# Optimization experiments

Hardware: AMD Instinct MI355X
Metric: run time of the kernel (lower is better)

## Reference

```python
import jax, jax.numpy as jnp
import numpy as np

B, L, D = 32, 256, 1024
ALIGN = 1024
FF = 2048
NUM_CLASSES = 3


def setup_inputs() -> dict:
    key = jax.random.key(0)
    ks = jax.random.split(key, 10)
    u = lambda k, shape: jax.random.uniform(k, shape, jnp.float32, -1.0, 1.0)
    return {
        "premises": jax.random.normal(ks[0], (B, L, D), jnp.float32),
        "hypotheses": jax.random.normal(ks[1], (B, L, D), jnp.float32),
        "W_F": u(ks[2], (D, ALIGN)),
        "W_G": u(ks[3], (2 * D, FF)),
        "W1": u(ks[4], (2 * FF, FF)) * 0.02,
        "b1": jnp.zeros((FF,), jnp.float32),
        "W2": u(ks[5], (FF, FF)) * 0.02,
        "b2": jnp.zeros((FF,), jnp.float32),
        "W3": u(ks[6], (FF, NUM_CLASSES)) * 0.02,
        "b3": jnp.zeros((NUM_CLASSES,), jnp.float32),
    }


def reference(premises, hypotheses, W_F, W_G, W1, b1, W2, b2, W3, b3):
    # ---- align: tanh-projected cross attention ----
    F_p = jnp.tanh(jnp.einsum("bpd,da->bpa", premises, W_F))      # [B,Lp,A]
    F_h = jnp.tanh(jnp.einsum("bhd,da->bha", hypotheses, W_F))    # [B,Lh,A]
    eijs = jnp.einsum("bpa,bha->bph", F_p, F_h)                   # [B,Lp,Lh]
    attn = jax.nn.softmax(eijs, axis=-1)                          # tf.nn.softmax: last axis
    betas = jnp.einsum("bph,bhd->bpd", attn, hypotheses)          # [B,Lp,D]
    alphas = jnp.einsum("bph,bpd->bhd", attn, premises)           # [B,Lh,D]

    # ---- compare (dropout is identity: p_keep = 1.0 at eval) ----
    V1 = jnp.tanh(jnp.concatenate([premises, betas], axis=2) @ W_G)    # [B,Lp,FF]
    V2 = jnp.tanh(jnp.concatenate([hypotheses, alphas], axis=2) @ W_G) # [B,Lh,FF]

    # ---- aggregate: sum-pool over sequence, concat ----
    agg = jnp.concatenate([V1.sum(axis=1), V2.sum(axis=1)], axis=1)    # [B,2*FF]

    # ---- classifier MLP ----
    a1 = jnp.tanh(agg @ W1 + b1)
    a2 = jnp.tanh(a1 @ W2 + b2)
    logits = a2 @ W3 + b3                                              # [B,3]
    return logits
```

## Files before the change

kernel.cpp:

```cpp
#include <hip/hip_runtime.h>
#include <hip/hip_bf16.h>
#include <stdint.h>


typedef __attribute__((ext_vector_type(8))) short    short8_t;
typedef __attribute__((ext_vector_type(4))) float    float4_t;
typedef __attribute__((ext_vector_type(8))) _Float16 half8_t;
typedef __attribute__((ext_vector_type(4))) _Float16 half4_t;
typedef __attribute__((ext_vector_type(2))) _Float16 half2_t;

#define DEVI static __device__ __forceinline__

DEVI short f2bf(float f) {
  union { float f; unsigned u; } v; v.f = f;
  unsigned r = v.u + 0x7fffu + ((v.u >> 16) & 1u);
  return (short)(r >> 16);
}
DEVI float bf2f(short s) {
  union { unsigned u; float f; } v;
  v.u = ((unsigned)(unsigned short)s) << 16;
  return v.f;
}
DEVI void split2(float x, short& hi, short& lo) {
  hi = f2bf(x);
  lo = f2bf(x - bf2f(hi));
}
DEVI float fast_tanh(float x) {
  float e = __expf(2.0f * x);
  return 1.0f - 2.0f / (e + 1.0f);
}
DEVI void gload16(const void* g, void* l) {
  __builtin_amdgcn_global_load_lds(
      (const __attribute__((address_space(1))) void*)g,
      (__attribute__((address_space(3))) void*)l, 16, 0, 0);
}

__global__ __launch_bounds__(512, 2) void gemm_split_f(
    const short* __restrict__ Ah, const short* __restrict__ Al,
    const short* __restrict__ Bh, const short* __restrict__ Bl,
    short* __restrict__ Fh, short* __restrict__ Fl)
{
  __shared__ __align__(16) short LDS[3][24576];

  const int id   = blockIdx.x;
  const int row0 = (id >> 2) * 128;
  const int col0 = (id & 3) * 256;
  const int tid  = threadIdx.x;
  const int lane = tid & 63, wave = tid >> 6;
  const int wr = wave >> 2, wc = wave & 3;
  const int m15 = lane & 15, q = lane >> 4;
  const int nt = 1024 / 32;

  const int cg = ((lane & 3) ^ ((lane >> 3) & 3)) * 8;
  const short* gptr[6];
  int ldsoff[6];
#pragma unroll
  for (int c = 0; c < 6; ++c) {
    const int f0 = wave * 96 + c * 16;
    const int fr = f0 + (lane >> 2);
    const short* base;
    size_t roff;
    if (f0 < 128)      { base = Ah; roff = (size_t)(row0 + fr) * 1024; }
    else if (f0 < 256) { base = Al; roff = (size_t)(row0 + fr - 128) * 1024; }
    else if (f0 < 512) { base = Bh; roff = (size_t)(col0 + fr - 256) * 1024; }
    else               { base = Bl; roff = (size_t)(col0 + fr - 512) * 1024; }
    gptr[c]   = base + roff + cg;
    ldsoff[c] = f0 * 32;
  }
  auto stage = [&](short* slotbase, int kt) {
#pragma unroll
    for (int c = 0; c < 6; ++c)
      gload16(gptr[c] + kt * 32, slotbase + ldsoff[c]);
  };

  const int xq = (q ^ ((m15 >> 1) & 3)) * 8;
  int arow[4], brow[4];
#pragma unroll
  for (int i = 0; i < 4; ++i) {
    arow[i] = (wr * 64 + i * 16 + m15) * 32 + xq;
    brow[i] = 8192 + (wc * 64 + i * 16 + m15) * 32 + xq;
  }

  float4_t acc[4][4];
#pragma unroll
  for (int i = 0; i < 4; ++i)
#pragma unroll
    for (int j = 0; j < 4; ++j) acc[i][j] = (float4_t)0.0f;

  stage(&LDS[0][0], 0);
  stage(&LDS[1][0], 1);
  asm volatile("s_waitcnt vmcnt(6)");
  __builtin_amdgcn_s_barrier();

  int cur = 0, st2 = 2;
  for (int t = 0; t < nt; ++t) {
    short* buf = &LDS[cur][0];
    __builtin_amdgcn_sched_barrier(0);

    short8_t ah[4], al[4], bh[4], bl[4];
#pragma unroll
    for (int i = 0; i < 4; ++i) {
      ah[i] = *(const short8_t*)&buf[arow[i]];
      al[i] = *(const short8_t*)&buf[arow[i] + 4096];
    }
#pragma unroll
    for (int j = 0; j < 4; ++j) {
      bh[j] = *(const short8_t*)&buf[brow[j]];
      bl[j] = *(const short8_t*)&buf[brow[j] + 8192];
    }

    if (t + 2 < nt) stage(&LDS[st2][0], t + 2);

    __builtin_amdgcn_s_setprio(1);
#pragma unroll
    for (int i = 0; i < 4; ++i)
#pragma unroll
      for (int j = 0; j < 4; ++j) {
        acc[i][j] = __builtin_amdgcn_mfma_f32_16x16x32_bf16(ah[i], bh[j], acc[i][j], 0, 0, 0);
        acc[i][j] = __builtin_amdgcn_mfma_f32_16x16x32_bf16(ah[i], bl[j], acc[i][j], 0, 0, 0);
        acc[i][j] = __builtin_amdgcn_mfma_f32_16x16x32_bf16(al[i], bh[j], acc[i][j], 0, 0, 0);
      }
    __builtin_amdgcn_s_setprio(0);

    __builtin_amdgcn_sched_barrier(0);
    if (t + 2 < nt) {
      asm volatile("s_waitcnt vmcnt(6)");
    } else if (t + 1 < nt) {
      asm volatile("s_waitcnt vmcnt(0)");
    }
    __builtin_amdgcn_s_barrier();
    cur = (cur == 2) ? 0 : cur + 1;
    st2 = (st2 == 2) ? 0 : st2 + 1;
  }

#pragma unroll
  for (int i = 0; i < 4; ++i) {
#pragma unroll
    for (int r = 0; r < 4; ++r) {
      const int gm = row0 + wr * 64 + i * 16 + q * 4 + r;
#pragma unroll
      for (int j = 0; j < 4; ++j) {
        const int gn = col0 + wc * 64 + j * 16 + m15;
        float v = fast_tanh(acc[i][j][r]);
        short hi, lo; split2(v, hi, lo);
        Fh[(size_t)gm * 1024 + gn] = hi;
        Fl[(size_t)gm * 1024 + gn] = lo;
      }
    }
  }
}

template <int DO_TANH, int OUT_MODE>
__global__ __launch_bounds__(256) void gemm_nt_split(
    const short* __restrict__ Ah, const short* __restrict__ Al, int lda, long sA,
    const short* __restrict__ Bh, const short* __restrict__ Bl, int ldb, long sB,
    void* __restrict__ Ch, void* __restrict__ Cl, int ldc, long sC,
    int M, int K, int kslices)
{
  __shared__ __align__(16) short Ash[128 * 32];
  __shared__ __align__(16) short Asl[128 * 32];
  __shared__ __align__(16) short Bsh[128 * 32];
  __shared__ __align__(16) short Bsl[128 * 32];

  const int z  = blockIdx.z;
  const int zb = z / kslices;
  const int Ksub = K / kslices;
  const int zk = z - zb * kslices;
  const int kbeg = zk * Ksub, kend = kbeg + Ksub;

  Ah += (size_t)zb * sA;  Al += (size_t)zb * sA;
  Bh += (size_t)zb * sB;  Bl += (size_t)zb * sB;

  const int row0 = blockIdx.x * 128;
  const int col0 = blockIdx.y * 128;

  const int t    = threadIdx.x;
  const int lane = t & 63;
  const int wave = t >> 6;
  const int wr = wave >> 1, wc = wave & 1;
  const int m15 = lane & 15, q = lane >> 4;

  const int schk = ((t & 3) ^ ((t >> 3) & 3)) * 8;
  const short* pAh = Ah + (size_t)(row0 + (t >> 2)) * lda + kbeg + schk;
  const short* pAl = Al + (size_t)(row0 + (t >> 2)) * lda + kbeg + schk;
  const short* pBh = Bh + (size_t)(col0 + (t >> 2)) * ldb + kbeg + schk;
  const short* pBl = Bl + (size_t)(col0 + (t >> 2)) * ldb + kbeg + schk;
  const size_t a64 = (size_t)64 * lda, b64 = (size_t)64 * ldb;
  short* lAh = &Ash[wave * 512];
  short* lAl = &Asl[wave * 512];
  short* lBh = &Bsh[wave * 512];
  short* lBl = &Bsl[wave * 512];

  const int fs2 = (q ^ ((m15 >> 1) & 3)) * 8;

  float4_t acc[4][4];
#pragma unroll
  for (int i = 0; i < 4; ++i)
#pragma unroll
    for (int j = 0; j < 4; ++j) acc[i][j] = (float4_t)0.0f;

  for (int k0 = kbeg; k0 < kend; k0 += 32) {
    gload16(pAh, lAh);  gload16(pAh + a64, lAh + 2048);
    gload16(pAl, lAl);  gload16(pAl + a64, lAl + 2048);
    gload16(pBh, lBh);  gload16(pBh + b64, lBh + 2048);
    gload16(pBl, lBl);  gload16(pBl + b64, lBl + 2048);
    pAh += 32; pAl += 32; pBh += 32; pBl += 32;
    __syncthreads();

    short8_t ah[4], al[4];
#pragma unroll
    for (int i = 0; i < 4; ++i) {
      const int ra = (wr * 64 + i * 16 + m15) * 32 + fs2;
      ah[i] = *(const short8_t*)&Ash[ra];
      al[i] = *(const short8_t*)&Asl[ra];
    }
#pragma unroll
    for (int j = 0; j < 4; ++j) {
      const int rb = (wc * 64 + j * 16 + m15) * 32 + fs2;
      short8_t bh = *(const short8_t*)&Bsh[rb];
      short8_t bl = *(const short8_t*)&Bsl[rb];
#pragma unroll
      for (int i = 0; i < 4; ++i) {
        acc[i][j] = __builtin_amdgcn_mfma_f32_16x16x32_bf16(ah[i], bh, acc[i][j], 0, 0, 0);
        acc[i][j] = __builtin_amdgcn_mfma_f32_16x16x32_bf16(ah[i], bl, acc[i][j], 0, 0, 0);
        acc[i][j] = __builtin_amdgcn_mfma_f32_16x16x32_bf16(al[i], bh, acc[i][j], 0, 0, 0);
      }
    }
    __syncthreads();
  }

  short* Chs = (short*)Ch + (size_t)zb * sC;
  short* Cls = (short*)Cl + (size_t)zb * sC;
  float* Cf  = (float*)Ch + (size_t)(OUT_MODE == 2 ? z : zb) * sC;
#pragma unroll
  for (int i = 0; i < 4; ++i) {
#pragma unroll
    for (int r = 0; r < 4; ++r) {
      int gm = row0 + wr * 64 + i * 16 + q * 4 + r;
      if (gm < M) {
#pragma unroll
        for (int j = 0; j < 4; ++j) {
          int gn = col0 + wc * 64 + j * 16 + m15;
          float v = acc[i][j][r];
          if (DO_TANH) v = fast_tanh(v);
          if (OUT_MODE == 2) {
            Cf[(size_t)gm * ldc + gn] = v;
          } else {
            short hi, lo; split2(v, hi, lo);
            Chs[(size_t)gm * ldc + gn] = hi;
            Cls[(size_t)gm * ldc + gn] = lo;
          }
        }
      }
    }
  }
}

__global__ __launch_bounds__(256) void gemm_f16(
    const _Float16* __restrict__ A, int lda, long sA,
    const _Float16* __restrict__ B, int ldb, long sB,
    _Float16* __restrict__ C, int ldc, long sC,
    int K, int bxor)
{
  __shared__ __align__(16) _Float16 As[2 * 128 * 32];
  __shared__ __align__(16) _Float16 Bs[2 * 128 * 32];

  const int z = blockIdx.z;
  A += (size_t)z * sA;
  B += (size_t)(z ^ bxor) * sB;

  const int row0 = blockIdx.x * 128;
  const int col0 = blockIdx.y * 128;
  const int t = threadIdx.x, lane = t & 63, wave = t >> 6;
  const int wr = wave >> 1, wc = wave & 1;
  const int m15 = lane & 15, q = lane >> 4;

  const int srow = wave * 32 + (lane >> 2);
  const int cg   = ((lane & 3) ^ ((lane >> 3) & 3)) * 8;
  const _Float16* gA0 = A + (size_t)(row0 + srow) * lda + cg;
  const _Float16* gA1 = gA0 + (size_t)16 * lda;
  const _Float16* gB0 = B + (size_t)(col0 + srow) * ldb + cg;
  const _Float16* gB1 = gB0 + (size_t)16 * ldb;
  const _Float16* gA0b = gA0 + 32;
  const _Float16* gA1b = gA1 + 32;
  const _Float16* gB0b = gB0 + 32;
  const _Float16* gB1b = gB1 + 32;
  _Float16* lA0  = &As[(wave * 32) * 32];
  _Float16* lA1  = &As[(wave * 32 + 16) * 32];
  _Float16* lB0  = &Bs[(wave * 32) * 32];
  _Float16* lB1  = &Bs[(wave * 32 + 16) * 32];
  _Float16* lA0b = lA0 + 4096;
  _Float16* lA1b = lA1 + 4096;
  _Float16* lB0b = lB0 + 4096;
  _Float16* lB1b = lB1 + 4096;

  const int fs = (q ^ ((m15 >> 1) & 3)) * 8;
  int aoff[4], boff[4];
#pragma unroll
  for (int i = 0; i < 4; ++i) {
    aoff[i] = (wr * 64 + i * 16 + m15) * 32 + fs;
    boff[i] = (wc * 64 + i * 16 + m15) * 32 + fs;
  }

  float4_t acc[4][4];
#pragma unroll
  for (int i = 0; i < 4; ++i)
#pragma unroll
    for (int j = 0; j < 4; ++j) acc[i][j] = (float4_t)0.0f;

  for (int k0 = 0; k0 < K; k0 += 64) {
    gload16(gA0, lA0);  gload16(gA1, lA1);
    gload16(gB0, lB0);  gload16(gB1, lB1);
    gload16(gA0b, lA0b); gload16(gA1b, lA1b);
    gload16(gB0b, lB0b); gload16(gB1b, lB1b);
    gA0 += 64; gA1 += 64; gB0 += 64; gB1 += 64;
    gA0b += 64; gA1b += 64; gB0b += 64; gB1b += 64;
    __syncthreads();

#pragma unroll
    for (int h = 0; h < 2; ++h) {
      half8_t af[4], bfr[4];
#pragma unroll
      for (int i = 0; i < 4; ++i) af[i]  = *(const half8_t*)&As[h * 4096 + aoff[i]];
#pragma unroll
      for (int j = 0; j < 4; ++j) bfr[j] = *(const half8_t*)&Bs[h * 4096 + boff[j]];
#pragma unroll
      for (int i = 0; i < 4; ++i)
#pragma unroll
        for (int j = 0; j < 4; ++j)
          acc[i][j] = __builtin_amdgcn_mfma_f32_16x16x32_f16(af[i], bfr[j], acc[i][j], 0, 0, 0);
    }
    __syncthreads();
  }

  {
    _Float16* Cp = C + (size_t)z * sC;
#pragma unroll
    for (int i = 0; i < 4; ++i)
#pragma unroll
      for (int r = 0; r < 4; ++r) {
        int gm = row0 + wr * 64 + i * 16 + q * 4 + r;
#pragma unroll
        for (int j = 0; j < 4; ++j) {
          int gn = col0 + wc * 64 + j * 16 + m15;
          Cp[(size_t)gm * ldc + gn] = (_Float16)acc[i][j][r];
        }
      }
  }
}

__global__ __launch_bounds__(512, 2) void gemm_f16_sum8(
    const _Float16* __restrict__ A, int lda,
    const _Float16* __restrict__ B, int ldb,
    int K, float* __restrict__ agg)
{
  __shared__ __align__(16) _Float16 LDS[4][2 * 256 * 32];

  const int row0 = blockIdx.x * 256;
  const int col0 = blockIdx.y * 256;
  const int tid  = threadIdx.x;
  const int lane = tid & 63, wave = tid >> 6;
  const int wr = wave >> 2, wc = wave & 3;
  const int m15 = lane & 15, q = lane >> 4;
  const int nt = K / 32;

  const int srow = wave * 32 + (lane >> 2);
  const int cg   = ((lane & 3) ^ ((lane >> 3) & 3)) * 8;
  const _Float16* gA = A + (size_t)(row0 + srow) * lda + cg;
  const _Float16* gB = B + (size_t)(col0 + srow) * ldb + cg;

  auto stageA = [&](int t) {
    const _Float16* g = gA + t * 32;
    _Float16* l = &LDS[t & 3][wave * 1024];
    gload16(g, l);
    gload16(g + (size_t)16 * lda, l + 512);
  };
  auto stageB = [&](int t) {
    const _Float16* g = gB + t * 32;
    _Float16* l = &LDS[t & 3][8192 + wave * 1024];
    gload16(g, l);
    gload16(g + (size_t)16 * ldb, l + 512);
  };

  const int xq = (q ^ ((m15 >> 1) & 3)) * 8;
  int aoff[8], boff[4];
#pragma unroll
  for (int i = 0; i < 8; ++i)
    aoff[i] = (wr * 128 + i * 16 + m15) * 32 + xq;
#pragma unroll
  for (int j = 0; j < 4; ++j)
    boff[j] = 8192 + (wc * 64 + j * 16 + m15) * 32 + xq;

  float4_t acc[8][4];
#pragma unroll
  for (int i = 0; i < 8; ++i)
#pragma unroll
    for (int j = 0; j < 4; ++j) acc[i][j] = (float4_t)0.0f;

  stageA(0); stageB(0);
  stageA(1); stageB(1);
  asm volatile("s_waitcnt vmcnt(4)");
  __builtin_amdgcn_s_barrier();

  for (int t = 0; t < nt; ++t) {
    const _Float16* buf = &LDS[t & 3][0];
    __builtin_amdgcn_sched_barrier(0);

    half8_t a0[4], a1[4], bb[4];
#pragma unroll
    for (int i = 0; i < 4; ++i) a0[i] = *(const half8_t*)&buf[aoff[i]];
#pragma unroll
    for (int j = 0; j < 4; ++j) bb[j] = *(const half8_t*)&buf[boff[j]];
#pragma unroll
    for (int i = 0; i < 4; ++i) a1[i] = *(const half8_t*)&buf[aoff[4 + i]];

    if (t + 2 < nt) { stageA(t + 2); stageB(t + 2); }

    __builtin_amdgcn_s_setprio(1);
#pragma unroll
    for (int i = 0; i < 4; ++i)
#pragma unroll
      for (int j = 0; j < 4; ++j)
        acc[i][j] = __builtin_amdgcn_mfma_f32_16x16x32_f16(a0[i], bb[j], acc[i][j], 0, 0, 0);
#pragma unroll
    for (int i = 0; i < 4; ++i)
#pragma unroll
      for (int j = 0; j < 4; ++j)
        acc[4 + i][j] = __builtin_amdgcn_mfma_f32_16x16x32_f16(a1[i], bb[j], acc[4 + i][j], 0, 0, 0);
    __builtin_amdgcn_s_setprio(0);

    __builtin_amdgcn_sched_barrier(0);
    if (t + 2 < nt) {
      asm volatile("s_waitcnt vmcnt(4)");
    } else if (t + 1 < nt) {
      asm volatile("s_waitcnt vmcnt(0)");
    }
    __builtin_amdgcn_s_barrier();
  }

  const int half_ = row0 >= 8192;
  const int b     = (row0 & 8191) >> 8;
#pragma unroll
  for (int j = 0; j < 4; ++j) {
    float s = 0.0f;
#pragma unroll
    for (int i = 0; i < 8; ++i)
#pragma unroll
      for (int r = 0; r < 4; ++r) s += fast_tanh(acc[i][j][r]);
    s += __shfl_xor(s, 16);
    s += __shfl_xor(s, 32);
    if (q == 0) {
      int col = col0 + wc * 64 + j * 16 + m15;
      atomicAdd(&agg[(size_t)b * 4096 + half_ * 2048 + col], s);
    }
  }
}

__global__ __launch_bounds__(256) void transpose_w(
    const float* __restrict__ WF, short* __restrict__ oh, short* __restrict__ ol,
    const float* __restrict__ WG, _Float16* __restrict__ og)
{
  __shared__ float tile[32][33];
  const int id = blockIdx.x;
  const int tx = threadIdx.x & 31, ty = threadIdx.x >> 5;
  if (id < 1024) {
    const int c0 = (id & 31) * 32, r0 = (id >> 5) * 32;
#pragma unroll
    for (int i = 0; i < 4; ++i) {
      int r = ty + i * 8;
      tile[r][tx] = WF[(size_t)(r0 + r) * 1024 + c0 + tx];
    }
    __syncthreads();
#pragma unroll
    for (int i = 0; i < 4; ++i) {
      int cc = ty + i * 8;
      float v = tile[tx][cc];
      short hi, lo; split2(v, hi, lo);
      size_t o = (size_t)(c0 + cc) * 1024 + r0 + tx;
      oh[o] = hi;
      ol[o] = lo;
    }
  } else {
    const int t2 = id - 1024;
    const int c0 = (t2 & 63) * 32, r0 = (t2 >> 6) * 32;
#pragma unroll
    for (int i = 0; i < 4; ++i) {
      int r = ty + i * 8;
      tile[r][tx] = WG[(size_t)(r0 + r) * 2048 + c0 + tx];
    }
    __syncthreads();
#pragma unroll
    for (int i = 0; i < 4; ++i) {
      int cc = ty + i * 8;
      og[(size_t)(c0 + cc) * 2048 + r0 + tx] = (_Float16)tile[tx][cc];
    }
  }
}

__global__ __launch_bounds__(256) void transpose_b2b(
    const short* __restrict__ in, short* __restrict__ out,
    int R, int C, long sIn, long sOut)
{
  __shared__ short tile[32][33];
  in  += (size_t)blockIdx.z * sIn;
  out += (size_t)blockIdx.z * sOut;
  const int tx = threadIdx.x & 31, ty = threadIdx.x >> 5;
  const int c0 = blockIdx.x * 32, r0 = blockIdx.y * 32;
#pragma unroll
  for (int i = 0; i < 4; ++i) {
    int r = ty + i * 8;
    tile[r][tx] = in[(size_t)(r0 + r) * C + c0 + tx];
  }
  __syncthreads();
#pragma unroll
  for (int i = 0; i < 4; ++i) {
    int cc = ty + i * 8;
    out[(size_t)(c0 + cc) * R + r0 + tx] = tile[tx][cc];
  }
}

__global__ __launch_bounds__(256) void conv_in_t(
    const float* __restrict__ P, const float* __restrict__ Hh,
    short* __restrict__ oh, short* __restrict__ ol,
    _Float16* __restrict__ cat, _Float16* __restrict__ phbt,
    float* __restrict__ agg)
{
  __shared__ __align__(16) float tile[64][68];
  const int zb   = blockIdx.z;
  const int half = zb >> 5, b = zb & 31;
  const int bid = (zb * 4 + blockIdx.y) * 16 + blockIdx.x;
  if (bid < 128) {
    float4_t zz = (float4_t)0.0f;
    *(float4_t*)&agg[(size_t)bid * 1024 + threadIdx.x * 4] = zz;
  }
  const float* in = (half ? Hh : P) + (size_t)b * 256 * 1024;
  const int c0 = blockIdx.x * 64;
  const int r0 = blockIdx.y * 64;
  const int t  = threadIdx.x;
  const int rl = t >> 4;
  const int c4 = (t & 15) * 4;
  const size_t rowbase = (size_t)half * 8192 + (size_t)b * 256;
#pragma unroll
  for (int i = 0; i < 4; ++i) {
    int r = rl + i * 16;
    float4 v = *(const float4*)&in[(size_t)(r0 + r) * 1024 + c0 + c4];
    *(float4*)&tile[r][c4] = v;
    short4 h, l;
    split2(v.x, h.x, l.x); split2(v.y, h.y, l.y);
    split2(v.z, h.z, l.z); split2(v.w, h.w, l.w);
    size_t o = (rowbase + r0 + r) * 1024 + c0 + c4;
    *(short4*)&oh[o] = h;
    *(short4*)&ol[o] = l;
    half4_t c16;
    c16.x = (_Float16)v.x; c16.y = (_Float16)v.y;
    c16.z = (_Float16)v.z; c16.w = (_Float16)v.w;
    *(half4_t*)&cat[(rowbase + r0 + r) * 2048 + c0 + c4] = c16;
  }
  __syncthreads();
  _Float16* op = phbt + (size_t)zb * 1024 * 256;
  const int tx = t & 31;
  const int w  = t >> 5;
#pragma unroll
  for (int i = 0; i < 8; ++i) {
    int cc = w + i * 8;
    half2_t p;
    p.x = (_Float16)tile[tx * 2][cc];
    p.y = (_Float16)tile[tx * 2 + 1][cc];
    *(half2_t*)&op[(size_t)(c0 + cc) * 256 + r0 + tx * 2] = p;
  }
}

__global__ __launch_bounds__(256) void softmax_rows(
    const float* __restrict__ e, _Float16* __restrict__ attn)
{
  const int row  = blockIdx.x * 4 + (threadIdx.x >> 6);
  const int lane = threadIdx.x & 63;
  const size_t base = ((size_t)(row >> 8) * 4) * 65536
                    + (size_t)(row & 255) * 256 + lane * 4;
  const float4 v0 = *(const float4*)&e[base];
  const float4 v1 = *(const float4*)&e[base + 65536];
  const float4 v2 = *(const float4*)&e[base + 2 * 65536];
  const float4 v3 = *(const float4*)&e[base + 3 * 65536];
  float4 v;
  v.x = (v0.x + v1.x) + (v2.x + v3.x);
  v.y = (v0.y + v1.y) + (v2.y + v3.y);
  v.z = (v0.z + v1.z) + (v2.z + v3.z);
  v.w = (v0.w + v1.w) + (v2.w + v3.w);
  float m = fmaxf(fmaxf(v.x, v.y), fmaxf(v.z, v.w));
#pragma unroll
  for (int off = 32; off; off >>= 1) m = fmaxf(m, __shfl_xor(m, off));
  float e0 = __expf(v.x - m), e1 = __expf(v.y - m);
  float e2 = __expf(v.z - m), e3 = __expf(v.w - m);
  float s = e0 + e1 + e2 + e3;
#pragma unroll
  for (int off = 32; off; off >>= 1) s += __shfl_xor(s, off);
  float inv = 1.0f / s;
  half4_t o;
  o.x = (_Float16)(e0 * inv); o.y = (_Float16)(e1 * inv);
  o.z = (_Float16)(e2 * inv); o.w = (_Float16)(e3 * inv);
  *(half4_t*)&attn[(size_t)row * 256 + lane * 4] = o;
}

__global__ __launch_bounds__(256) void skinny_gemm(
    const float* __restrict__ A, const float* __restrict__ B,
    float* __restrict__ outp, int N, int K)
{
  __shared__ float Asl[256][33];
  const int n0 = blockIdx.x * 64;
  const int k0 = blockIdx.y * 256;
  const int t  = threadIdx.x;
#pragma unroll
  for (int j = 0; j < 32; ++j) {
    Asl[t][j] = A[(size_t)j * K + k0 + t];
  }
  __syncthreads();
  const int l = t & 63, w = t >> 6;
  const int n = n0 + l;
  float acc[8] = {0.f, 0.f, 0.f, 0.f, 0.f, 0.f, 0.f, 0.f};
  const float* Bp = B + (size_t)k0 * N + n;
#pragma unroll 4
  for (int k = 0; k < 256; ++k) {
    float bv = Bp[(size_t)k * N];
#pragma unroll
    for (int m = 0; m < 8; ++m)
      acc[m] += Asl[k][w * 8 + m] * bv;
  }
  float* o = outp + (size_t)blockIdx.y * 32 * N;
#pragma unroll
  for (int m = 0; m < 8; ++m)
    o[(size_t)(w * 8 + m) * N + n] = acc[m];
}

__global__ __launch_bounds__(256) void bias_sum_tanh(
    const float* __restrict__ parts, int nslice,
    const float* __restrict__ bias, float* __restrict__ o, int n)
{
  int i = blockIdx.x * 256 + threadIdx.x;
  if (i < n) {
    float s = 0.0f;
    for (int sl = 0; sl < nslice; ++sl) s += parts[(size_t)sl * n + i];
    o[i] = fast_tanh(s + bias[i & 2047]);
  }
}

__global__ __launch_bounds__(256) void logits2(
    const float* __restrict__ c2parts, const float* __restrict__ b2,
    const float* __restrict__ W3, const float* __restrict__ b3,
    float* __restrict__ out)
{
  const int b = blockIdx.x, t = threadIdx.x;
  float p0 = 0.f, p1 = 0.f, p2 = 0.f;
  for (int k = t; k < 2048; k += 256) {
    float c = 0.0f;
#pragma unroll
    for (int sl = 0; sl < 8; ++sl) c += c2parts[(size_t)sl * 65536 + b * 2048 + k];
    float a = fast_tanh(c + b2[k]);
    p0 += a * W3[k * 3 + 0];
    p1 += a * W3[k * 3 + 1];
    p2 += a * W3[k * 3 + 2];
  }
#pragma unroll
  for (int off = 32; off; off >>= 1) {
    p0 += __shfl_xor(p0, off);
    p1 += __shfl_xor(p1, off);
    p2 += __shfl_xor(p2, off);
  }
  __shared__ float red[4][3];
  if ((t & 63) == 0) {
    red[t >> 6][0] = p0; red[t >> 6][1] = p1; red[t >> 6][2] = p2;
  }
  __syncthreads();
  if (t < 3) out[b * 3 + t] = b3[t] + red[0][t] + red[1][t] + red[2][t] + red[3][t];
}

extern "C" void kernel_launch(void* const* d_in, const int* in_sizes, int n_in,
                              void* d_out, int out_size, void* d_ws, size_t ws_size,
                              hipStream_t stream) {
  (void)in_sizes; (void)n_in; (void)out_size; (void)ws_size;
  const float* P   = (const float*)d_in[0];
  const float* H   = (const float*)d_in[1];
  const float* W_F = (const float*)d_in[2];
  const float* W_G = (const float*)d_in[3];
  const float* W1  = (const float*)d_in[4];
  const float* b1  = (const float*)d_in[5];
  const float* W2  = (const float*)d_in[6];
  const float* b2  = (const float*)d_in[7];
  const float* W3  = (const float*)d_in[8];
  const float* b3  = (const float*)d_in[9];
  float* out = (float*)d_out;

  char* wsp = (char*)d_ws;
  auto alloc = [&](size_t bytes) {
    char* p = wsp;
    wsp += (bytes + 255) & ~(size_t)255;
    return p;
  };
  short*    Pp_h  = (short*)alloc(16384ull * 1024 * 2);
  short*    Pp_l  = (short*)alloc(16384ull * 1024 * 2);
  _Float16* Cat16 = (_Float16*)alloc(16384ull * 2048 * 2);
  short*    Fbuf  = (short*)alloc(32ull * 1024 * 1024 * 2);
  _Float16* PHbT  = (_Float16*)alloc(64ull * 1024 * 256 * 2);
  short*    WFT_h = (short*)alloc(1024ull * 1024 * 2);
  short*    WFT_l = (short*)alloc(1024ull * 1024 * 2);
  _Float16* WGT16 = (_Float16*)alloc(2048ull * 2048 * 2);
  _Float16* attn  = (_Float16*)alloc(32ull * 256 * 256 * 2);
  _Float16* attnT = (_Float16*)alloc(32ull * 256 * 256 * 2);
  float*    agg   = (float*)alloc(32ull * 4096 * 4);
  float*    a1f   = (float*)alloc(32ull * 2048 * 4);

  short* F_h = Fbuf;
  short* F_l = Fbuf + 16384ull * 1024;
  float* eparts  = (float*)Pp_h;
  float* c1parts = (float*)Pp_l;
  float* c2parts = (float*)(Pp_l + 4ull * 1024 * 1024);

  conv_in_t<<<dim3(16, 4, 64), 256, 0, stream>>>(P, H, Pp_h, Pp_l, Cat16, PHbT, agg);
  transpose_w<<<5120, 256, 0, stream>>>(W_F, WFT_h, WFT_l, W_G, WGT16);

  gemm_split_f<<<512, 512, 0, stream>>>(Pp_h, Pp_l, WFT_h, WFT_l, F_h, F_l);

  gemm_nt_split<0, 2><<<dim3(2, 2, 128), 256, 0, stream>>>(
      F_h, F_l, 1024, 256 * 1024,
      F_h + 8192ull * 1024, F_l + 8192ull * 1024, 1024, 256 * 1024,
      eparts, nullptr, 256, 65536, 256, 1024, 4);

  softmax_rows<<<2048, 256, 0, stream>>>(eparts, attn);
  transpose_b2b<<<dim3(8, 8, 32), 256, 0, stream>>>(
      (const short*)attn, (short*)attnT, 256, 256, 65536, 65536);

  gemm_f16<<<dim3(2, 8, 64), 256, 0, stream>>>(
      attn, 256, 65536, PHbT, 256, 1024 * 256,
      Cat16 + 1024, 2048, 256 * 2048, 256, 32);

  gemm_f16_sum8<<<dim3(64, 8, 1), 512, 0, stream>>>(
      Cat16, 2048, WGT16, 2048, 2048, agg);

  skinny_gemm<<<dim3(32, 16), 256, 0, stream>>>(agg, W1, c1parts, 2048, 4096);
  bias_sum_tanh<<<256, 256, 0, stream>>>(c1parts, 16, b1, a1f, 32 * 2048);
  skinny_gemm<<<dim3(32, 8), 256, 0, stream>>>(a1f, W2, c2parts, 2048, 2048);
  logits2<<<32, 256, 0, stream>>>(c2parts, b2, W3, b3, out);
}
```

Baseline: 547.4 us.

## Replace attention-score and attention-apply GEMMs with triple-buffered 512-thread kernels

Replaces the generic split-bf16 NT GEMM for the attention scores with a dedicated 512-thread kernel that uses a 128x256 tile and a three-slot LDS ring. Global loads for step t+2 are issued while MFMAs run on step t, with explicit vmcnt waits and setprio. The f16 GEMM that applies attention to the sequence inputs gets the same treatment, using 128x256 tiles and 8 waves. The intent is to hide global-load latency, cut barrier stalls, and reuse larger B tiles, at the cost of more LDS per block and hardcoded shapes.

```diff
diff --git a/kernel.cpp b/kernel.cpp
--- a/kernel.cpp
+++ b/kernel.cpp
@@ -150,48 +150,163 @@
   }
 }
 
-template <int DO_TANH, int OUT_MODE>
-__global__ __launch_bounds__(256) void gemm_nt_split(
-    const short* __restrict__ Ah, const short* __restrict__ Al, int lda, long sA,
-    const short* __restrict__ Bh, const short* __restrict__ Bl, int ldb, long sB,
-    void* __restrict__ Ch, void* __restrict__ Cl, int ldc, long sC,
-    int M, int K, int kslices)
-{
-  __shared__ __align__(16) short Ash[128 * 32];
-  __shared__ __align__(16) short Asl[128 * 32];
-  __shared__ __align__(16) short Bsh[128 * 32];
-  __shared__ __align__(16) short Bsl[128 * 32];
-
+__global__ __launch_bounds__(512, 2) void gemm_split_e(
+    const short* __restrict__ Fh, const short* __restrict__ Fl,
+    float* __restrict__ eparts)
+{
+  __shared__ __align__(16) short LDS[3][24576];
+
+  const int id = blockIdx.x;
+  const int zb = id >> 3;
+  const int sp = (id >> 2) & 1;
+  const int zk = id & 3;
+  const int arow0 = zb * 256 + sp * 128;
+  const int brow0 = 8192 + zb * 256;
+  const int kbeg  = zk * 256;
+  const int tid = threadIdx.x, lane = tid & 63, wave = tid >> 6;
+  const int wr = wave >> 2, wc = wave & 3;
+  const int m15 = lane & 15, q = lane >> 4;
+  const int nt = 8;
+
+  const int cg = ((lane & 3) ^ ((lane >> 3) & 3)) * 8;
+  const short* gptr[6];
+  int ldsoff[6];
+#pragma unroll
+  for (int c = 0; c < 6; ++c) {
+    const int f0 = wave * 96 + c * 16;
+    const int fr = f0 + (lane >> 2);
+    const short* base;
+    size_t roff;
+    if (f0 < 128)      { base = Fh; roff = (size_t)(arow0 + fr) * 1024; }
+    else if (f0 < 256) { base = Fl; roff = (size_t)(arow0 + fr - 128) * 1024; }
+    else if (f0 < 512) { base = Fh; roff = (size_t)(brow0 + fr - 256) * 1024; }
+    else               { base = Fl; roff = (size_t)(brow0 + fr - 512) * 1024; }
+    gptr[c]   = base + roff + kbeg + cg;
+    ldsoff[c] = f0 * 32;
+  }
+  auto stage = [&](short* slotbase, int kt) {
+#pragma unroll
+    for (int c = 0; c < 6; ++c)
+      gload16(gptr[c] + kt * 32, slotbase + ldsoff[c]);
+  };
+
+  const int xq = (q ^ ((m15 >> 1) & 3)) * 8;
+  int arow[4], brow[4];
+#pragma unroll
+  for (int i = 0; i < 4; ++i) {
+    arow[i] = (wr * 64 + i * 16 + m15) * 32 + xq;
+    brow[i] = 8192 + (wc * 64 + i * 16 + m15) * 32 + xq;
+  }
+
+  float4_t acc[4][4];
+#pragma unroll
+  for (int i = 0; i < 4; ++i)
+#pragma unroll
+    for (int j = 0; j < 4; ++j) acc[i][j] = (float4_t)0.0f;
+
+  stage(&LDS[0][0], 0);
+  stage(&LDS[1][0], 1);
+  asm volatile("s_waitcnt vmcnt(6)");
+  __builtin_amdgcn_s_barrier();
+
+  int cur = 0, st2 = 2;
+  for (int t = 0; t < nt; ++t) {
+    short* buf = &LDS[cur][0];
+    __builtin_amdgcn_sched_barrier(0);
+
+    short8_t ah[4], al[4], bh[4], bl[4];
+#pragma unroll
+    for (int i = 0; i < 4; ++i) {
+      ah[i] = *(const short8_t*)&buf[arow[i]];
+      al[i] = *(const short8_t*)&buf[arow[i] + 4096];
+    }
+#pragma unroll
+    for (int j = 0; j < 4; ++j) {
+      bh[j] = *(const short8_t*)&buf[brow[j]];
+      bl[j] = *(const short8_t*)&buf[brow[j] + 8192];
+    }
+
+    if (t + 2 < nt) stage(&LDS[st2][0], t + 2);
+
+    __builtin_amdgcn_s_setprio(1);
+#pragma unroll
+    for (int i = 0; i < 4; ++i)
+#pragma unroll
+      for (int j = 0; j < 4; ++j) {
+        acc[i][j] = __builtin_amdgcn_mfma_f32_16x16x32_bf16(ah[i], bh[j], acc[i][j], 0, 0, 0);
+        acc[i][j] = __builtin_amdgcn_mfma_f32_16x16x32_bf16(ah[i], bl[j], acc[i][j], 0, 0, 0);
+        acc[i][j] = __builtin_amdgcn_mfma_f32_16x16x32_bf16(al[i], bh[j], acc[i][j], 0, 0, 0);
+      }
+    __builtin_amdgcn_s_setprio(0);
+
+    __builtin_amdgcn_sched_barrier(0);
+    if (t + 2 < nt) {
+      asm volatile("s_waitcnt vmcnt(6)");
+    } else if (t + 1 < nt) {
+      asm volatile("s_waitcnt vmcnt(0)");
+    }
+    __builtin_amdgcn_s_barrier();
+    cur = (cur == 2) ? 0 : cur + 1;
+    st2 = (st2 == 2) ? 0 : st2 + 1;
+  }
+
+  float* ep = eparts + (size_t)(zb * 4 + zk) * 65536;
+#pragma unroll
+  for (int i = 0; i < 4; ++i) {
+#pragma unroll
+    for (int r = 0; r < 4; ++r) {
+      const int gm = sp * 128 + wr * 64 + i * 16 + q * 4 + r;
+#pragma unroll
+      for (int j = 0; j < 4; ++j) {
+        const int gn = wc * 64 + j * 16 + m15;
+        ep[(size_t)gm * 256 + gn] = acc[i][j][r];
+      }
+    }
+  }
+}
+
+__global__ __launch_bounds__(512, 2) void gemm_f16r(
+    const _Float16* __restrict__ attn, const _Float16* __restrict__ phbt,
+    _Float16* __restrict__ cat)
+{
+  __shared__ __align__(16) _Float16 LDS[3][12288];
+
+  const int bx = blockIdx.x;
   const int z  = blockIdx.z;
-  const int zb = z / kslices;
-  const int Ksub = K / kslices;
-  const int zk = z - zb * kslices;
-  const int kbeg = zk * Ksub, kend = kbeg + Ksub;
-
-  Ah += (size_t)zb * sA;  Al += (size_t)zb * sA;
-  Bh += (size_t)zb * sB;  Bl += (size_t)zb * sB;
-
-  const int row0 = blockIdx.x * 128;
-  const int col0 = blockIdx.y * 128;
-
-  const int t    = threadIdx.x;
-  const int lane = t & 63;
-  const int wave = t >> 6;
-  const int wr = wave >> 1, wc = wave & 1;
+  const int mt = bx >> 2, ntile = bx & 3;
+  const int row0 = mt * 128;
+  const int col0 = ntile * 256;
+  const _Float16* A = attn + (size_t)z * 65536;
+  const _Float16* B = phbt + (size_t)(z ^ 32) * 262144 + (size_t)col0 * 256;
+  const int tid = threadIdx.x, lane = tid & 63, wave = tid >> 6;
+  const int wr = wave >> 2, wc = wave & 3;
   const int m15 = lane & 15, q = lane >> 4;
-
-  const int schk = ((t & 3) ^ ((t >> 3) & 3)) * 8;
-  const short* pAh = Ah + (size_t)(row0 + (t >> 2)) * lda + kbeg + schk;
-  const short* pAl = Al + (size_t)(row0 + (t >> 2)) * lda + kbeg + schk;
-  const short* pBh = Bh + (size_t)(col0 + (t >> 2)) * ldb + kbeg + schk;
-  const short* pBl = Bl + (size_t)(col0 + (t >> 2)) * ldb + kbeg + schk;
-  const size_t a64 = (size_t)64 * lda, b64 = (size_t)64 * ldb;
-  short* lAh = &Ash[wave * 512];
-  short* lAl = &Asl[wave * 512];
-  short* lBh = &Bsh[wave * 512];
-  short* lBl = &Bsl[wave * 512];
-
-  const int fs2 = (q ^ ((m15 >> 1) & 3)) * 8;
+  const int nt = 8;
+
+  const int cg = ((lane & 3) ^ ((lane >> 3) & 3)) * 8;
+  const _Float16* gptr[3];
+  int ldsoff[3];
+#pragma unroll
+  for (int c = 0; c < 3; ++c) {
+    const int f0 = wave * 48 + c * 16;
+    const int fr = f0 + (lane >> 2);
+    if (f0 < 128) gptr[c] = A + (size_t)(row0 + fr) * 256 + cg;
+    else          gptr[c] = B + (size_t)(fr - 128) * 256 + cg;
+    ldsoff[c] = f0 * 32;
+  }
+  auto stage = [&](_Float16* slotbase, int kt) {
+#pragma unroll
+    for (int c = 0; c < 3; ++c)
+      gload16(gptr[c] + kt * 32, slotbase + ldsoff[c]);
+  };
+
+  const int xq = (q ^ ((m15 >> 1) & 3)) * 8;
+  int aoff[4], boff[4];
+#pragma unroll
+  for (int i = 0; i < 4; ++i) {
+    aoff[i] = (wr * 64 + i * 16 + m15) * 32 + xq;
+    boff[i] = (128 + wc * 64 + i * 16 + m15) * 32 + xq;
+  }
 
   float4_t acc[4][4];
 #pragma unroll
@@ -199,153 +314,55 @@
 #pragma unroll
     for (int j = 0; j < 4; ++j) acc[i][j] = (float4_t)0.0f;
 
-  for (int k0 = kbeg; k0 < kend; k0 += 32) {
-    gload16(pAh, lAh);  gload16(pAh + a64, lAh + 2048);
-    gload16(pAl, lAl);  gload16(pAl + a64, lAl + 2048);
-    gload16(pBh, lBh);  gload16(pBh + b64, lBh + 2048);
-    gload16(pBl, lBl);  gload16(pBl + b64, lBl + 2048);
-    pAh += 32; pAl += 32; pBh += 32; pBl += 32;
-    __syncthreads();
-
-    short8_t ah[4], al[4];
-#pragma unroll
-    for (int i = 0; i < 4; ++i) {
-      const int ra = (wr * 64 + i * 16 + m15) * 32 + fs2;
-      ah[i] = *(const short8_t*)&Ash[ra];
-      al[i] = *(const short8_t*)&Asl[ra];
-    }
-#pragma unroll
-    for (int j = 0; j < 4; ++j) {
-      const int rb = (wc * 64 + j * 16 + m15) * 32 + fs2;
-      short8_t bh = *(const short8_t*)&Bsh[rb];
-      short8_t bl = *(const short8_t*)&Bsl[rb];
-#pragma unroll
-      for (int i = 0; i < 4; ++i) {
-        acc[i][j] = __builtin_amdgcn_mfma_f32_16x16x32_bf16(ah[i], bh, acc[i][j], 0, 0, 0);
-        acc[i][j] = __builtin_amdgcn_mfma_f32_16x16x32_bf16(ah[i], bl, acc[i][j], 0, 0, 0);
-        acc[i][j] = __builtin_amdgcn_mfma_f32_16x16x32_bf16(al[i], bh, acc[i][j], 0, 0, 0);
+  stage(&LDS[0][0], 0);
+  stage(&LDS[1][0], 1);
+  asm volatile("s_waitcnt vmcnt(3)");
+  __builtin_amdgcn_s_barrier();
+
+  int cur = 0, st2 = 2;
+  for (int t = 0; t < nt; ++t) {
+    _Float16* buf = &LDS[cur][0];
+    __builtin_amdgcn_sched_barrier(0);
+
+    half8_t af[4], bf[4];
+#pragma unroll
+    for (int i = 0; i < 4; ++i) af[i] = *(const half8_t*)&buf[aoff[i]];
+#pragma unroll
+    for (int j = 0; j < 4; ++j) bf[j] = *(const half8_t*)&buf[boff[j]];
+
+    if (t + 2 < nt) stage(&LDS[st2][0], t + 2);
+
+    __builtin_amdgcn_s_setprio(1);
+#pragma unroll
+    for (int i = 0; i < 4; ++i)
+#pragma unroll
+      for (int j = 0; j < 4; ++j)
+        acc[i][j] = __builtin_amdgcn_mfma_f32_16x16x32_f16(af[i], bf[j], acc[i][j], 0, 0, 0);
+    __builtin_amdgcn_s_setprio(0);
+
+    __builtin_amdgcn_sched_barrier(0);
+    if (t + 2 < nt) {
+      asm volatile("s_waitcnt vmcnt(3)");
+    } else if (t + 1 < nt) {
+      asm volatile("s_waitcnt vmcnt(0)");
+    }
+    __builtin_amdgcn_s_barrier();
+    cur = (cur == 2) ? 0 : cur + 1;
+    st2 = (st2 == 2) ? 0 : st2 + 1;
+  }
+
+  _Float16* Cp = cat + 1024 + (size_t)z * (256 * 2048);
+#pragma unroll
+  for (int i = 0; i < 4; ++i) {
+#pragma unroll
+    for (int r = 0; r < 4; ++r) {
+      const int gm = row0 + wr * 64 + i * 16 + q * 4 + r;
+#pragma unroll
+      for (int j = 0; j < 4; ++j) {
+        const int gn = col0 + wc * 64 + j * 16 + m15;
+        Cp[(size_t)gm * 2048 + gn] = (_Float16)acc[i][j][r];
       }
     }
-    __syncthreads();
-  }
-
-  short* Chs = (short*)Ch + (size_t)zb * sC;
-  short* Cls = (short*)Cl + (size_t)zb * sC;
-  float* Cf  = (float*)Ch + (size_t)(OUT_MODE == 2 ? z : zb) * sC;
-#pragma unroll
-  for (int i = 0; i < 4; ++i) {
-#pragma unroll
-    for (int r = 0; r < 4; ++r) {
-      int gm = row0 + wr * 64 + i * 16 + q * 4 + r;
-      if (gm < M) {
-#pragma unroll
-        for (int j = 0; j < 4; ++j) {
-          int gn = col0 + wc * 64 + j * 16 + m15;
-          float v = acc[i][j][r];
-          if (DO_TANH) v = fast_tanh(v);
-          if (OUT_MODE == 2) {
-            Cf[(size_t)gm * ldc + gn] = v;
-          } else {
-            short hi, lo; split2(v, hi, lo);
-            Chs[(size_t)gm * ldc + gn] = hi;
-            Cls[(size_t)gm * ldc + gn] = lo;
-          }
-        }
-      }
-    }
-  }
-}
-
-__global__ __launch_bounds__(256) void gemm_f16(
-    const _Float16* __restrict__ A, int lda, long sA,
-    const _Float16* __restrict__ B, int ldb, long sB,
-    _Float16* __restrict__ C, int ldc, long sC,
-    int K, int bxor)
-{
-  __shared__ __align__(16) _Float16 As[2 * 128 * 32];
-  __shared__ __align__(16) _Float16 Bs[2 * 128 * 32];
-
-  const int z = blockIdx.z;
-  A += (size_t)z * sA;
-  B += (size_t)(z ^ bxor) * sB;
-
-  const int row0 = blockIdx.x * 128;
-  const int col0 = blockIdx.y * 128;
-  const int t = threadIdx.x, lane = t & 63, wave = t >> 6;
-  const int wr = wave >> 1, wc = wave & 1;
-  const int m15 = lane & 15, q = lane >> 4;
-
-  const int srow = wave * 32 + (lane >> 2);
-  const int cg   = ((lane & 3) ^ ((lane >> 3) & 3)) * 8;
-  const _Float16* gA0 = A + (size_t)(row0 + srow) * lda + cg;
-  const _Float16* gA1 = gA0 + (size_t)16 * lda;
-  const _Float16* gB0 = B + (size_t)(col0 + srow) * ldb + cg;
-  const _Float16* gB1 = gB0 + (size_t)16 * ldb;
-  const _Float16* gA0b = gA0 + 32;
-  const _Float16* gA1b = gA1 + 32;
-  const _Float16* gB0b = gB0 + 32;
-  const _Float16* gB1b = gB1 + 32;
-  _Float16* lA0  = &As[(wave * 32) * 32];
-  _Float16* lA1  = &As[(wave * 32 + 16) * 32];
-  _Float16* lB0  = &Bs[(wave * 32) * 32];
-  _Float16* lB1  = &Bs[(wave * 32 + 16) * 32];
-  _Float16* lA0b = lA0 + 4096;
-  _Float16* lA1b = lA1 + 4096;
-  _Float16* lB0b = lB0 + 4096;
-  _Float16* lB1b = lB1 + 4096;
-
-  const int fs = (q ^ ((m15 >> 1) & 3)) * 8;
-  int aoff[4], boff[4];
-#pragma unroll
-  for (int i = 0; i < 4; ++i) {
-    aoff[i] = (wr * 64 + i * 16 + m15) * 32 + fs;
-    boff[i] = (wc * 64 + i * 16 + m15) * 32 + fs;
-  }
-
-  float4_t acc[4][4];
-#pragma unroll
-  for (int i = 0; i < 4; ++i)
-#pragma unroll
-    for (int j = 0; j < 4; ++j) acc[i][j] = (float4_t)0.0f;
-
-  for (int k0 = 0; k0 < K; k0 += 64) {
-    gload16(gA0, lA0);  gload16(gA1, lA1);
-    gload16(gB0, lB0);  gload16(gB1, lB1);
-    gload16(gA0b, lA0b); gload16(gA1b, lA1b);
-    gload16(gB0b, lB0b); gload16(gB1b, lB1b);
-    gA0 += 64; gA1 += 64; gB0 += 64; gB1 += 64;
-    gA0b += 64; gA1b += 64; gB0b += 64; gB1b += 64;
-    __syncthreads();
-
-#pragma unroll
-    for (int h = 0; h < 2; ++h) {
-      half8_t af[4], bfr[4];
-#pragma unroll
-      for (int i = 0; i < 4; ++i) af[i]  = *(const half8_t*)&As[h * 4096 + aoff[i]];
-#pragma unroll
-      for (int j = 0; j < 4; ++j) bfr[j] = *(const half8_t*)&Bs[h * 4096 + boff[j]];
-#pragma unroll
-      for (int i = 0; i < 4; ++i)
-#pragma unroll
-        for (int j = 0; j < 4; ++j)
-          acc[i][j] = __builtin_amdgcn_mfma_f32_16x16x32_f16(af[i], bfr[j], acc[i][j], 0, 0, 0);
-    }
-    __syncthreads();
-  }
-
-  {
-    _Float16* Cp = C + (size_t)z * sC;
-#pragma unroll
-    for (int i = 0; i < 4; ++i)
-#pragma unroll
-      for (int r = 0; r < 4; ++r) {
-        int gm = row0 + wr * 64 + i * 16 + q * 4 + r;
-#pragma unroll
-        for (int j = 0; j < 4; ++j) {
-          int gn = col0 + wc * 64 + j * 16 + m15;
-          Cp[(size_t)gm * ldc + gn] = (_Float16)acc[i][j][r];
-        }
-      }
   }
 }
 
@@ -719,18 +736,13 @@
 
   gemm_split_f<<<512, 512, 0, stream>>>(Pp_h, Pp_l, WFT_h, WFT_l, F_h, F_l);
 
-  gemm_nt_split<0, 2><<<dim3(2, 2, 128), 256, 0, stream>>>(
-      F_h, F_l, 1024, 256 * 1024,
-      F_h + 8192ull * 1024, F_l + 8192ull * 1024, 1024, 256 * 1024,
-      eparts, nullptr, 256, 65536, 256, 1024, 4);
+  gemm_split_e<<<256, 512, 0, stream>>>(F_h, F_l, eparts);
 
   softmax_rows<<<2048, 256, 0, stream>>>(eparts, attn);
   transpose_b2b<<<dim3(8, 8, 32), 256, 0, stream>>>(
       (const short*)attn, (short*)attnT, 256, 256, 65536, 65536);
 
-  gemm_f16<<<dim3(2, 8, 64), 256, 0, stream>>>(
-      attn, 256, 65536, PHbT, 256, 1024 * 256,
-      Cat16 + 1024, 2048, 256 * 2048, 256, 32);
+  gemm_f16r<<<dim3(8, 1, 64), 512, 0, stream>>>(attn, PHbT, Cat16);
 
   gemm_f16_sum8<<<dim3(64, 8, 1), 512, 0, stream>>>(
       Cat16, 2048, WGT16, 2048, 2048, agg);
```

New measurement: 541.1 us (median of 2 runs). Within noise of the previous version (-1.1%).
